# Performance work log

Hardware: AMD Instinct MI355X
Metric: run time of the kernel (lower is better)

Reference implementation:

```python
import jax, jax.numpy as jnp
import numpy as np
import math

B, S, D, N, H = 4, 2048, 1024, 512, 8
HD = D // H  # head_dim = 128
LN_EPS = 1e-5


def setup_inputs() -> dict:
    key = jax.random.key(0)
    ks = jax.random.split(key, 12)
    return {
        "query": jax.random.normal(ks[0], (B, S, D), jnp.float32),
        "memory_weights": jax.random.uniform(ks[1], (B, S, N), jnp.float32),
        "update_input": jax.random.normal(ks[2], (B, S, D), jnp.float32),
        "memory_keys": jax.random.normal(ks[3], (N, D), jnp.float32),
        "memory_values": jax.random.normal(ks[4], (N, D), jnp.float32),
        "memory_decay": jnp.float32(0.95),
        "gate_w": jax.random.normal(ks[5], (2 * D, D), jnp.float32) / math.sqrt(2 * D),
        "gate_b": jnp.zeros((D,), jnp.float32),
        "out_w": jax.random.normal(ks[6], (D, D), jnp.float32) / math.sqrt(D),
        "out_b": jnp.zeros((D,), jnp.float32),
        "ln_gamma": jnp.ones((D,), jnp.float32),
        "ln_beta": jnp.zeros((D,), jnp.float32),
    }


def reference(query, memory_weights, update_input, memory_keys, memory_values,
              memory_decay, gate_w, gate_b, out_w, out_b, ln_gamma, ln_beta):
    # Multi-head attention read: einsum 'bshd,nhd->bsn' sums over h and d,
    # so it equals a full [D]-dot product; only the scale uses head_dim.
    scores = jnp.einsum("bsd,nd->bsn", query, memory_keys) / math.sqrt(HD)
    scores = scores * memory_weights  # multiplicative mask before softmax
    probs = jax.nn.softmax(scores, axis=-1)
    memory_read = jnp.einsum("bsn,nd->bsd", probs, memory_values)
    memory_read = memory_read * memory_decay

    # Gated update path (update_input provided)
    gate_in = jnp.concatenate([memory_read, update_input], axis=-1)  # [B,S,2D]
    gate = jax.nn.sigmoid(gate_in @ gate_w + gate_b)  # [B,S,D]
    # NOTE: the no_grad EMA update of memory_values is a side effect that does
    # not influence this forward output; omitted from the pure reference.
    memory_read = memory_read * (1.0 + jnp.mean(gate, axis=-1, keepdims=True))

    out = memory_read @ out_w + out_b  # output projection (dropout = eval identity)
    mu = jnp.mean(out, axis=-1, keepdims=True)
    var = jnp.var(out, axis=-1, keepdims=True)
    out = (out - mu) * jax.lax.rsqrt(var + LN_EPS) * ln_gamma + ln_beta
    return out
```

## Files before the change

kernel.cpp:

```cpp
#include <hip/hip_runtime.h>
#include <hip/hip_bf16.h>

typedef __attribute__((ext_vector_type(8))) short bf16x8;
typedef __attribute__((ext_vector_type(4))) float f32x4;
typedef __attribute__((ext_vector_type(4))) int i32x4;
typedef __attribute__((ext_vector_type(2))) int i32x2;
typedef __attribute__((ext_vector_type(4))) unsigned short u16x4;

static __device__ __forceinline__ void gload_lds16(const void* g, void* l) {
  __builtin_amdgcn_global_load_lds((const __attribute__((address_space(1))) void*)g,
                                   (__attribute__((address_space(3))) void*)l,
                                   16, 0, 0);
}

static __device__ __forceinline__ unsigned short f2bf(float x) {
  unsigned int u = __float_as_uint(x);
  u += 0x7fffu + ((u >> 16) & 1u);
  return (unsigned short)(u >> 16);
}
static __device__ __forceinline__ float bf2f(unsigned short u) {
  return __uint_as_float((unsigned int)u << 16);
}

template <int BM, int BN, int NT>
static __device__ __forceinline__ void gemm_core(
    const unsigned short* __restrict__ A, int lda,
    const unsigned short* __restrict__ Bt, int ldb,
    int kbeg, int kend, int brow, int bcol,
    unsigned short* As, unsigned short* Bs,
    f32x4 (&acc)[BM / (8 * (NT / 64))][BN / 32])
{
  constexpr int NW = NT / 64;
  constexpr int MA = BM / (8 * NW), NB = BN / 32;
  constexpr int CA = 8 * BM / NT, CB = 8 * BN / NT;
  const int tid = threadIdx.x;
  const int wid = tid >> 6, lane = tid & 63;
  const int wr = wid >> 1, wc = wid & 1;
  const int l15 = lane & 15, l4 = lane >> 4;
  const int foff = tid * 8;

  for (int k0 = kbeg; k0 < kend; k0 += 64) {
#pragma unroll
    for (int c = 0; c < CA; ++c) {
      int f = c * (NT * 8) + foff;
      gload_lds16(A + (size_t)(brow + (f >> 6)) * lda + k0 + (f & 63), As + f);
    }
#pragma unroll
    for (int c = 0; c < CB; ++c) {
      int f = c * (NT * 8) + foff;
      gload_lds16(Bt + (size_t)(bcol + (f >> 6)) * ldb + k0 + (f & 63), Bs + f);
    }
    __syncthreads();
#pragma unroll
    for (int kk = 0; kk < 2; ++kk) {
      const int ko = kk * 32 + l4 * 8;
      bf16x8 af[MA], bfv[NB];
#pragma unroll
      for (int m = 0; m < MA; ++m)
        af[m] = *(const bf16x8*)(As + (wr * (16 * MA) + m * 16 + l15) * 64 + ko);
#pragma unroll
      for (int n = 0; n < NB; ++n)
        bfv[n] = *(const bf16x8*)(Bs + (wc * (BN / 2) + n * 16 + l15) * 64 + ko);
#pragma unroll
      for (int m = 0; m < MA; ++m)
#pragma unroll
        for (int n = 0; n < NB; ++n)
          acc[m][n] = __builtin_amdgcn_mfma_f32_16x16x32_bf16(af[m], bfv[n], acc[m][n], 0, 0, 0);
    }
    __syncthreads();
  }
}

__global__ __launch_bounds__(256)
void prep(const float* __restrict__ ob, int* __restrict__ flag,
          float* __restrict__ zeros,
          const float* __restrict__ mk, const float* __restrict__ mv,
          unsigned short* __restrict__ kb, unsigned short* __restrict__ mvb,
          const float* __restrict__ ow, unsigned short* __restrict__ owt,
          const float* __restrict__ q, unsigned short* __restrict__ qb,
          const float* __restrict__ upd, unsigned short* __restrict__ cat,
          const float* __restrict__ gw, unsigned short* __restrict__ gwt,
          unsigned short* __restrict__ vt)
{
  __shared__ float t[32][33];
  const int b = blockIdx.x;
  const int tid = threadIdx.x;
  if (b == 0) {
    f32x4 v = *(const f32x4*)(ob + tid * 4);
    float mx = fmaxf(fmaxf(fabsf(v[0]), fabsf(v[1])), fmaxf(fabsf(v[2]), fabsf(v[3])));
#pragma unroll
    for (int off = 32; off >= 1; off >>= 1) mx = fmaxf(mx, __shfl_xor(mx, off, 64));
    __shared__ float sm[4];
    const int wid = tid >> 6, lane = tid & 63;
    if (lane == 0) sm[wid] = mx;
    __syncthreads();
    if (tid == 0) {
      float m = fmaxf(fmaxf(sm[0], sm[1]), fmaxf(sm[2], sm[3]));
      *flag = (m != 0.0f) ? 1 : 0;
    }
  } else if (b < 17) {
    f32x4 z = {};
    *(f32x4*)(zeros + (b - 1) * 1024 + tid * 4) = z;
  } else if (b < 529) {
    int idx = (b - 17) * 256 + tid;
    const float* in; unsigned short* out; int rel;
    if (idx < 65536) { in = mk; out = kb;  rel = idx; }
    else             { in = mv; out = mvb; rel = idx - 65536; }
    size_t f = (size_t)rel * 8;
    f32x4 a = *(const f32x4*)(in + f);
    f32x4 c = *(const f32x4*)(in + f + 4);
    union { unsigned short u[8]; i32x4 vec; } pk;
#pragma unroll
    for (int i = 0; i < 4; ++i) { pk.u[i] = f2bf(a[i]); pk.u[4 + i] = f2bf(c[i]); }
    *(i32x4*)(out + f) = pk.vec;
  } else if (b < 1553) {
    int id = b - 529;
    const int bx = id & 31, by = id >> 5;
    const int tx = tid & 31, ty = tid >> 5;
    const int c0 = bx * 32, r0 = by * 32;
#pragma unroll
    for (int i = 0; i < 4; ++i)
      t[ty + i * 8][tx] = ow[(size_t)(r0 + ty + i * 8) * 1024 + c0 + tx];
    __syncthreads();
#pragma unroll
    for (int i = 0; i < 4; ++i)
      owt[(size_t)(c0 + ty + i * 8) * 1024 + r0 + tx] = f2bf(t[tx][ty + i * 8]);
  } else if (b < 5649) {
    int idx = (b - 1553) * 256 + tid;
    size_t f = (size_t)idx * 8;
    f32x4 a = *(const f32x4*)(q + f);
    f32x4 c = *(const f32x4*)(q + f + 4);
    union { unsigned short u[8]; i32x4 vec; } pk;
#pragma unroll
    for (int i = 0; i < 4; ++i) { pk.u[i] = f2bf(a[i]); pk.u[4 + i] = f2bf(c[i]); }
    *(i32x4*)(qb + f) = pk.vec;
  } else {
    f32x4 v = *(const f32x4*)(ob + tid * 4);
    float mx = fmaxf(fmaxf(fabsf(v[0]), fabsf(v[1])), fmaxf(fabsf(v[2]), fabsf(v[3])));
#pragma unroll
    for (int off = 32; off >= 1; off >>= 1) mx = fmaxf(mx, __shfl_xor(mx, off, 64));
    __shared__ float sm2[4];
    const int wid = tid >> 6, lane = tid & 63;
    if (lane == 0) sm2[wid] = mx;
    __syncthreads();
    float m = fmaxf(fmaxf(sm2[0], sm2[1]), fmaxf(sm2[2], sm2[3]));
    if (m == 0.0f) return;
    __syncthreads();
    int g = b - 5649;
    if (g < 4096) {
      int idx = g * 256 + tid;
      size_t f = (size_t)idx * 8;
      int row = (int)(f >> 10);
      int col = (int)(f & 1023);
      f32x4 a = *(const f32x4*)(upd + f);
      f32x4 c = *(const f32x4*)(upd + f + 4);
      union { unsigned short u[8]; i32x4 vec; } pk;
#pragma unroll
      for (int i = 0; i < 4; ++i) { pk.u[i] = f2bf(a[i]); pk.u[4 + i] = f2bf(c[i]); }
      *(i32x4*)(cat + (size_t)row * 2048 + 1024 + col) = pk.vec;
    } else {
      const float* in; unsigned short* out; int R, id;
      if (g < 6144) { in = gw; out = gwt; R = 2048; id = g - 4096; }
      else          { in = mv; out = vt;  R = 512;  id = g - 6144; }
      const int bx = id & 31, by = id >> 5;
      const int tx = tid & 31, ty = tid >> 5;
      const int c0 = bx * 32, r0 = by * 32;
#pragma unroll
      for (int i = 0; i < 4; ++i)
        t[ty + i * 8][tx] = in[(size_t)(r0 + ty + i * 8) * 1024 + c0 + tx];
      __syncthreads();
#pragma unroll
      for (int i = 0; i < 4; ++i)
        out[(size_t)(c0 + ty + i * 8) * R + r0 + tx] = f2bf(t[tx][ty + i * 8]);
    }
  }
}

__global__ __launch_bounds__(512, 8)
void k_scores_w2(const unsigned short* __restrict__ qb,
                 const unsigned short* __restrict__ kb,
                 const float* __restrict__ mw,
                 unsigned short* __restrict__ probs,
                 const unsigned short* __restrict__ owt,
                 const unsigned short* __restrict__ mvb,
                 float* __restrict__ w2p)
{
  __shared__ unsigned short As[128 * 64];
  __shared__ unsigned short Bs[64 * 64];
  const int b = blockIdx.x;
  const int tid = threadIdx.x;
  const int wid = tid >> 6, lane = tid & 63;
  const int wr = wid >> 1, wc = wid & 1;
  const int l15 = lane & 15, l4 = lane >> 4;

  if (b < 512) {
    const int swz = (b & 7) * 64 + (b >> 3);
    const int bx = swz & 7, by = swz >> 3;
    const int brow = by * 128, bcol = bx * 64;
    f32x4 acc[2][2] = {};
    gemm_core<128, 64, 512>(qb, 1024, kb, 1024, 0, 1024, brow, bcol, As, Bs, acc);

#pragma unroll
    for (int m = 0; m < 2; ++m) {
#pragma unroll
      for (int j = 0; j < 4; ++j) {
        int row = brow + wr * 32 + m * 16 + l4 * 4 + j;
        const float* mwrow = mw + (size_t)row * 512;
#pragma unroll
        for (int n = 0; n < 2; ++n) {
          int col = bcol + wc * 32 + n * 16 + l15;
          float p = __expf(acc[m][n][j] * 0.08838834764831845f * mwrow[col]);
          float o = __shfl_xor(p, 1);
          if (!(lane & 1)) {
            unsigned int pw = (unsigned int)f2bf(p) | ((unsigned int)f2bf(o) << 16);
            *(unsigned int*)(probs + (size_t)row * 512 + col) = pw;
          }
        }
      }
    }
  } else {
    const int g = b - 512;
    const int bx = g & 7;
    const int by = (g >> 3) & 7;
    const int bz = g >> 6;
    const int brow = by * 128, bcol = bx * 64;
    f32x4 acc[2][2] = {};
    gemm_core<128, 64, 512>(owt, 1024, mvb, 1024, bz * 512, bz * 512 + 512,
                            brow, bcol, As, Bs, acc);
    float* dst = w2p + (size_t)bz * 524288;
#pragma unroll
    for (int m = 0; m < 2; ++m) {
      int row0 = brow + wr * 32 + m * 16 + l4 * 4;
#pragma unroll
      for (int j = 0; j < 4; ++j) {
#pragma unroll
        for (int n = 0; n < 2; ++n)
          dst[(size_t)(row0 + j) * 512 + bcol + wc * 32 + n * 16 + l15] = acc[m][n][j];
      }
    }
  }
}

__global__ __launch_bounds__(256)
void k_w2red_rowsum(const float* __restrict__ w2p, unsigned short* __restrict__ w2t,
                    const float* __restrict__ dec,
                    const unsigned short* __restrict__ probs,
                    float* __restrict__ rowsum,
                    const int* __restrict__ flag)
{
  const int b = blockIdx.x;
  const int tid = threadIdx.x;
  if (b < 512) {
    const int i = (b * 256 + tid) * 4;
    const float d = *dec;
    f32x4 s0 = *(const f32x4*)(w2p + i);
    f32x4 s1 = *(const f32x4*)(w2p + 524288 + i);
    union { unsigned short u[4]; i32x2 v; } pk;
#pragma unroll
    for (int j = 0; j < 4; ++j) pk.u[j] = f2bf((s0[j] + s1[j]) * d);
    *(i32x2*)(w2t + i) = pk.v;
  } else {
    if (*flag == 0) return;
    const int wid = tid >> 6, lane = tid & 63;
    const int row = (b - 512) * 4 + wid;
    bf16x8 v = *(const bf16x8*)(probs + (size_t)row * 512 + lane * 8);
    float s = 0.0f;
#pragma unroll
    for (int i = 0; i < 8; ++i) s += bf2f((unsigned short)v[i]);
#pragma unroll
    for (int off = 32; off >= 1; off >>= 1) s += __shfl_xor(s, off, 64);
    if (lane == 0) rowsum[row] = s;
  }
}

__global__ __launch_bounds__(512)
void k_out_read(const unsigned short* __restrict__ probs,
                const unsigned short* __restrict__ w2t,
                const float* __restrict__ rowsum,
                unsigned short* __restrict__ outpre,
                const unsigned short* __restrict__ vt,
                unsigned short* __restrict__ cat,
                const float* __restrict__ dec,
                const int* __restrict__ flag)
{
  __shared__ unsigned short As[128 * 64];
  __shared__ unsigned short Bs[128 * 64];
  const int b = blockIdx.x;
  const int tid = threadIdx.x;
  const int wid = tid >> 6, lane = tid & 63;
  const int wr = wid >> 1, wc = wid & 1;
  const int l15 = lane & 15, l4 = lane >> 4;

  if (b < 512) {
    const int swz = (b & 7) * 64 + (b >> 3);
    const int bx = swz & 7, by = swz >> 3;
    const int brow = by * 128, bcol = bx * 128;
    f32x4 acc[2][4] = {};
    gemm_core<128, 128, 512>(probs, 512, w2t, 512, 0, 512, brow, bcol, As, Bs, acc);
    const bool nf = (*flag != 0);
#pragma unroll
    for (int m = 0; m < 2; ++m) {
      int row0 = brow + wr * 32 + m * 16 + l4 * 4;
#pragma unroll
      for (int j = 0; j < 4; ++j) {
        int row = row0 + j;
        const float rscl = nf ? (1.0f / rowsum[row]) : 1.0f;
#pragma unroll
        for (int n = 0; n < 4; ++n) {
          int col = bcol + wc * 64 + n * 16 + l15;
          float v = acc[m][n][j] * rscl;
          float o = __shfl_xor(v, 1);
          if (!(lane & 1)) {
            unsigned int pw = (unsigned int)f2bf(v) | ((unsigned int)f2bf(o) << 16);
            *(unsigned int*)(outpre + (size_t)row * 1024 + col) = pw;
          }
        }
      }
    }
  } else {
    if (*flag == 0) return;
    const int f = b - 512;
    const int swz = (f & 7) * 64 + (f >> 3);
    const int bx = swz & 7, by = swz >> 3;
    const int brow = by * 128, bcol = bx * 128;
    f32x4 acc[2][4] = {};
    gemm_core<128, 128, 512>(probs, 512, vt, 512, 0, 512, brow, bcol, As, Bs, acc);
    const float d = *dec;
#pragma unroll
    for (int m = 0; m < 2; ++m) {
      int row0 = brow + wr * 32 + m * 16 + l4 * 4;
#pragma unroll
      for (int j = 0; j < 4; ++j) {
        int row = row0 + j;
        const float rscl = d / rowsum[row];
#pragma unroll
        for (int n = 0; n < 4; ++n) {
          int col = bcol + wc * 64 + n * 16 + l15;
          cat[(size_t)row * 2048 + col] = f2bf(acc[m][n][j] * rscl);
        }
      }
    }
  }
}

__global__ __launch_bounds__(256)
void k_gate(const unsigned short* __restrict__ cat,
            const unsigned short* __restrict__ gwt,
            const float* __restrict__ gb,
            float* __restrict__ gsum,
            const int* __restrict__ flag)
{
  if (*flag == 0) return;
  __shared__ unsigned short As[128 * 64];
  __shared__ unsigned short Bs[128 * 64];
  const int b = blockIdx.x;
  const int tid = threadIdx.x;
  const int wid = tid >> 6, lane = tid & 63;
  const int wr = wid >> 1, wc = wid & 1;
  const int l15 = lane & 15, l4 = lane >> 4;
  const int swz = (b & 7) * 64 + (b >> 3);
  const int bx = swz & 7, by = swz >> 3;
  const int brow = by * 128, bcol = bx * 128;
  f32x4 acc[4][4] = {};
  gemm_core<128, 128, 256>(cat, 2048, gwt, 2048, 0, 2048, brow, bcol, As, Bs, acc);
#pragma unroll
  for (int m = 0; m < 4; ++m) {
#pragma unroll
    for (int j = 0; j < 4; ++j) {
      float part = 0.0f;
#pragma unroll
      for (int n = 0; n < 4; ++n) {
        int col = bcol + wc * 64 + n * 16 + l15;
        float x = acc[m][n][j] + gb[col];
        part += 1.0f / (1.0f + __expf(-x));
      }
#pragma unroll
      for (int off = 1; off < 16; off <<= 1)
        part += __shfl_xor(part, off, 64);
      if (l15 == 0) {
        int row = brow + wr * 64 + m * 16 + l4 * 4 + j;
        atomicAdd(&gsum[row], part);
      }
    }
  }
}

__global__ __launch_bounds__(256)
void ln_rows(const unsigned short* __restrict__ X, const float* __restrict__ gsum,
             const float* __restrict__ ob,
             const float* __restrict__ gamma, const float* __restrict__ beta,
             float* __restrict__ Y)
{
  const int row = blockIdx.x;
  const int tid = threadIdx.x;
  const size_t base = (size_t)row * 1024 + tid * 4;
  const float scl = 1.0f + gsum[row] * (1.0f / 1024.0f);
  u16x4 xr = *(const u16x4*)(X + base);
  f32x4 bo = *(const f32x4*)(ob + tid * 4);
  float x[4];
#pragma unroll
  for (int i = 0; i < 4; ++i) x[i] = bf2f(xr[i]) * scl + bo[i];
  float s = x[0] + x[1] + x[2] + x[3];
  float q = x[0] * x[0] + x[1] * x[1] + x[2] * x[2] + x[3] * x[3];
#pragma unroll
  for (int off = 32; off >= 1; off >>= 1) {
    s += __shfl_xor(s, off, 64);
    q += __shfl_xor(q, off, 64);
  }
  __shared__ float ss[4], qq[4];
  const int wid = tid >> 6, lane = tid & 63;
  if (lane == 0) { ss[wid] = s; qq[wid] = q; }
  __syncthreads();
  s = ss[0] + ss[1] + ss[2] + ss[3];
  q = qq[0] + qq[1] + qq[2] + qq[3];
  const float mu = s * (1.0f / 1024.0f);
  const float var = q * (1.0f / 1024.0f) - mu * mu;
  const float r = rsqrtf(var + 1e-5f);
  f32x4 g = *(const f32x4*)(gamma + tid * 4);
  f32x4 bt = *(const f32x4*)(beta + tid * 4);
  f32x4 y;
#pragma unroll
  for (int i = 0; i < 4; ++i) y[i] = (x[i] - mu) * r * g[i] + bt[i];
  *(f32x4*)(Y + base) = y;
}

extern "C" void kernel_launch(void* const* d_in, const int* in_sizes, int n_in,
                              void* d_out, int out_size, void* d_ws, size_t ws_size,
                              hipStream_t stream)
{
  (void)in_sizes; (void)n_in; (void)out_size; (void)ws_size;
  const float* q   = (const float*)d_in[0];
  const float* mw  = (const float*)d_in[1];
  const float* upd = (const float*)d_in[2];
  const float* mk  = (const float*)d_in[3];
  const float* mv  = (const float*)d_in[4];
  const float* dec = (const float*)d_in[5];
  const float* gw  = (const float*)d_in[6];
  const float* gb  = (const float*)d_in[7];
  const float* ow  = (const float*)d_in[8];
  const float* ob  = (const float*)d_in[9];
  const float* lg  = (const float*)d_in[10];
  const float* lb  = (const float*)d_in[11];
  float* outp = (float*)d_out;
  char* ws = (char*)d_ws;

  unsigned short* qb     = (unsigned short*)(ws + 0);
  unsigned short* probs  = (unsigned short*)(ws + 16777216);
  unsigned short* outpre = (unsigned short*)(ws + 25165824);
  unsigned short* kb     = (unsigned short*)(ws + 41943040);
  unsigned short* mvb    = (unsigned short*)(ws + 42991616);
  unsigned short* owt    = (unsigned short*)(ws + 44040192);
  unsigned short* w2t    = (unsigned short*)(ws + 46137344);
  float*          w2p    = (float*)(ws + 47185920);
  unsigned short* vt     = (unsigned short*)(ws + 51380224);
  unsigned short* gwt    = (unsigned short*)(ws + 52428800);
  unsigned short* cat    = (unsigned short*)(ws + 56623104);
  float*          gsum   = (float*)(ws + 90177536);
  float*          rowsum = (float*)(ws + 90210304);
  int*            flag   = (int*)(ws + 90243072);

  prep<<<12305, 256, 0, stream>>>(ob, flag, gsum, mk, mv, kb, mvb, ow, owt,
                                  q, qb, upd, cat, gw, gwt, vt);
  k_scores_w2<<<640, 512, 0, stream>>>(qb, kb, mw, probs, owt, mvb, w2p);
  k_w2red_rowsum<<<2560, 256, 0, stream>>>(w2p, w2t, dec, probs, rowsum, flag);
  k_out_read<<<1024, 512, 0, stream>>>(probs, w2t, rowsum, outpre, vt, cat, dec, flag);
  k_gate<<<512, 256, 0, stream>>>(cat, gwt, gb, gsum, flag);
  ln_rows<<<8192, 256, 0, stream>>>(outpre, gsum, ob, lg, lb, outp);
}
```

Before: 77.49 us.

## Drop split-K W2 reduction kernel, fuse rowsum into output GEMM, warp-per-row LayerNorm

The W2 = out_w^T·mem_values GEMM now runs over the full K range in 64 blocks instead of split-K into two fp32 partials. The decay-scaled bf16 result is written straight from the epilogue, which removes the separate reduction kernel and its launch. The probs row sums are recomputed inside each k_out_read block into shared memory rather than read from a global buffer. That adds redundant reads of probs (each row is summed by 8 column blocks). LayerNorm is restructured to one wavefront per row, removing the shared-memory reduction and block barrier.

```diff
diff --git a/kernel.cpp b/kernel.cpp
--- a/kernel.cpp
+++ b/kernel.cpp
@@ -5,7 +5,6 @@
 typedef __attribute__((ext_vector_type(4))) float f32x4;
 typedef __attribute__((ext_vector_type(4))) int i32x4;
 typedef __attribute__((ext_vector_type(2))) int i32x2;
-typedef __attribute__((ext_vector_type(4))) unsigned short u16x4;
 
 static __device__ __forceinline__ void gload_lds16(const void* g, void* l) {
   __builtin_amdgcn_global_load_lds((const __attribute__((address_space(1))) void*)g,
@@ -183,7 +182,8 @@
                  unsigned short* __restrict__ probs,
                  const unsigned short* __restrict__ owt,
                  const unsigned short* __restrict__ mvb,
-                 float* __restrict__ w2p)
+                 unsigned short* __restrict__ w2t,
+                 const float* __restrict__ dec)
 {
   __shared__ unsigned short As[128 * 64];
   __shared__ unsigned short Bs[64 * 64];
@@ -221,62 +221,34 @@
   } else {
     const int g = b - 512;
     const int bx = g & 7;
-    const int by = (g >> 3) & 7;
-    const int bz = g >> 6;
+    const int by = g >> 3;
     const int brow = by * 128, bcol = bx * 64;
     f32x4 acc[2][2] = {};
-    gemm_core<128, 64, 512>(owt, 1024, mvb, 1024, bz * 512, bz * 512 + 512,
-                            brow, bcol, As, Bs, acc);
-    float* dst = w2p + (size_t)bz * 524288;
+    gemm_core<128, 64, 512>(owt, 1024, mvb, 1024, 0, 1024, brow, bcol, As, Bs, acc);
+    const float d = *dec;
 #pragma unroll
     for (int m = 0; m < 2; ++m) {
-      int row0 = brow + wr * 32 + m * 16 + l4 * 4;
 #pragma unroll
       for (int j = 0; j < 4; ++j) {
-#pragma unroll
-        for (int n = 0; n < 2; ++n)
-          dst[(size_t)(row0 + j) * 512 + bcol + wc * 32 + n * 16 + l15] = acc[m][n][j];
-      }
-    }
-  }
-}
-
-__global__ __launch_bounds__(256)
-void k_w2red_rowsum(const float* __restrict__ w2p, unsigned short* __restrict__ w2t,
-                    const float* __restrict__ dec,
-                    const unsigned short* __restrict__ probs,
-                    float* __restrict__ rowsum,
-                    const int* __restrict__ flag)
-{
-  const int b = blockIdx.x;
-  const int tid = threadIdx.x;
-  if (b < 512) {
-    const int i = (b * 256 + tid) * 4;
-    const float d = *dec;
-    f32x4 s0 = *(const f32x4*)(w2p + i);
-    f32x4 s1 = *(const f32x4*)(w2p + 524288 + i);
-    union { unsigned short u[4]; i32x2 v; } pk;
-#pragma unroll
-    for (int j = 0; j < 4; ++j) pk.u[j] = f2bf((s0[j] + s1[j]) * d);
-    *(i32x2*)(w2t + i) = pk.v;
-  } else {
-    if (*flag == 0) return;
-    const int wid = tid >> 6, lane = tid & 63;
-    const int row = (b - 512) * 4 + wid;
-    bf16x8 v = *(const bf16x8*)(probs + (size_t)row * 512 + lane * 8);
-    float s = 0.0f;
-#pragma unroll
-    for (int i = 0; i < 8; ++i) s += bf2f((unsigned short)v[i]);
-#pragma unroll
-    for (int off = 32; off >= 1; off >>= 1) s += __shfl_xor(s, off, 64);
-    if (lane == 0) rowsum[row] = s;
+        int row = brow + wr * 32 + m * 16 + l4 * 4 + j;
+#pragma unroll
+        for (int n = 0; n < 2; ++n) {
+          int col = bcol + wc * 32 + n * 16 + l15;
+          float v = acc[m][n][j] * d;
+          float o = __shfl_xor(v, 1);
+          if (!(lane & 1)) {
+            unsigned int pw = (unsigned int)f2bf(v) | ((unsigned int)f2bf(o) << 16);
+            *(unsigned int*)(w2t + (size_t)row * 512 + col) = pw;
+          }
+        }
+      }
+    }
   }
 }
 
 __global__ __launch_bounds__(512)
 void k_out_read(const unsigned short* __restrict__ probs,
                 const unsigned short* __restrict__ w2t,
-                const float* __restrict__ rowsum,
                 unsigned short* __restrict__ outpre,
                 const unsigned short* __restrict__ vt,
                 unsigned short* __restrict__ cat,
@@ -285,11 +257,13 @@
 {
   __shared__ unsigned short As[128 * 64];
   __shared__ unsigned short Bs[128 * 64];
+  __shared__ float srow[128];
   const int b = blockIdx.x;
   const int tid = threadIdx.x;
   const int wid = tid >> 6, lane = tid & 63;
   const int wr = wid >> 1, wc = wid & 1;
   const int l15 = lane & 15, l4 = lane >> 4;
+  const bool nf = (*flag != 0);
 
   if (b < 512) {
     const int swz = (b & 7) * 64 + (b >> 3);
@@ -297,14 +271,26 @@
     const int brow = by * 128, bcol = bx * 128;
     f32x4 acc[2][4] = {};
     gemm_core<128, 128, 512>(probs, 512, w2t, 512, 0, 512, brow, bcol, As, Bs, acc);
-    const bool nf = (*flag != 0);
+    if (nf) {
+      for (int r = 0; r < 16; ++r) {
+        int row = brow + wid * 16 + r;
+        bf16x8 v = *(const bf16x8*)(probs + (size_t)row * 512 + lane * 8);
+        float s = 0.0f;
+#pragma unroll
+        for (int i = 0; i < 8; ++i) s += bf2f((unsigned short)v[i]);
+#pragma unroll
+        for (int off = 32; off >= 1; off >>= 1) s += __shfl_xor(s, off, 64);
+        if (lane == 0) srow[wid * 16 + r] = s;
+      }
+      __syncthreads();
+    }
 #pragma unroll
     for (int m = 0; m < 2; ++m) {
       int row0 = brow + wr * 32 + m * 16 + l4 * 4;
 #pragma unroll
       for (int j = 0; j < 4; ++j) {
         int row = row0 + j;
-        const float rscl = nf ? (1.0f / rowsum[row]) : 1.0f;
+        const float rscl = nf ? (1.0f / srow[row - brow]) : 1.0f;
 #pragma unroll
         for (int n = 0; n < 4; ++n) {
           int col = bcol + wc * 64 + n * 16 + l15;
@@ -318,13 +304,24 @@
       }
     }
   } else {
-    if (*flag == 0) return;
+    if (!nf) return;
     const int f = b - 512;
     const int swz = (f & 7) * 64 + (f >> 3);
     const int bx = swz & 7, by = swz >> 3;
     const int brow = by * 128, bcol = bx * 128;
     f32x4 acc[2][4] = {};
     gemm_core<128, 128, 512>(probs, 512, vt, 512, 0, 512, brow, bcol, As, Bs, acc);
+    for (int r = 0; r < 16; ++r) {
+      int row = brow + wid * 16 + r;
+      bf16x8 v = *(const bf16x8*)(probs + (size_t)row * 512 + lane * 8);
+      float s = 0.0f;
+#pragma unroll
+      for (int i = 0; i < 8; ++i) s += bf2f((unsigned short)v[i]);
+#pragma unroll
+      for (int off = 32; off >= 1; off >>= 1) s += __shfl_xor(s, off, 64);
+      if (lane == 0) srow[wid * 16 + r] = s;
+    }
+    __syncthreads();
     const float d = *dec;
 #pragma unroll
     for (int m = 0; m < 2; ++m) {
@@ -332,7 +329,7 @@
 #pragma unroll
       for (int j = 0; j < 4; ++j) {
         int row = row0 + j;
-        const float rscl = d / rowsum[row];
+        const float rscl = d / srow[row - brow];
 #pragma unroll
         for (int n = 0; n < 4; ++n) {
           int col = bcol + wc * 64 + n * 16 + l15;
@@ -391,37 +388,40 @@
              const float* __restrict__ gamma, const float* __restrict__ beta,
              float* __restrict__ Y)
 {
-  const int row = blockIdx.x;
-  const int tid = threadIdx.x;
-  const size_t base = (size_t)row * 1024 + tid * 4;
+  const int wid = threadIdx.x >> 6, lane = threadIdx.x & 63;
+  const int row = blockIdx.x * 4 + wid;
+  const size_t base = (size_t)row * 1024 + lane * 16;
+  const int cb = lane * 16;
   const float scl = 1.0f + gsum[row] * (1.0f / 1024.0f);
-  u16x4 xr = *(const u16x4*)(X + base);
-  f32x4 bo = *(const f32x4*)(ob + tid * 4);
-  float x[4];
-#pragma unroll
-  for (int i = 0; i < 4; ++i) x[i] = bf2f(xr[i]) * scl + bo[i];
-  float s = x[0] + x[1] + x[2] + x[3];
-  float q = x[0] * x[0] + x[1] * x[1] + x[2] * x[2] + x[3] * x[3];
+  bf16x8 x0 = *(const bf16x8*)(X + base);
+  bf16x8 x1 = *(const bf16x8*)(X + base + 8);
+  float x[16];
+#pragma unroll
+  for (int i = 0; i < 8; ++i) {
+    x[i]     = bf2f((unsigned short)x0[i]) * scl + ob[cb + i];
+    x[8 + i] = bf2f((unsigned short)x1[i]) * scl + ob[cb + 8 + i];
+  }
+  float s = 0.0f, qsum = 0.0f;
+#pragma unroll
+  for (int i = 0; i < 16; ++i) { s += x[i]; qsum += x[i] * x[i]; }
 #pragma unroll
   for (int off = 32; off >= 1; off >>= 1) {
     s += __shfl_xor(s, off, 64);
-    q += __shfl_xor(q, off, 64);
-  }
-  __shared__ float ss[4], qq[4];
-  const int wid = tid >> 6, lane = tid & 63;
-  if (lane == 0) { ss[wid] = s; qq[wid] = q; }
-  __syncthreads();
-  s = ss[0] + ss[1] + ss[2] + ss[3];
-  q = qq[0] + qq[1] + qq[2] + qq[3];
+    qsum += __shfl_xor(qsum, off, 64);
+  }
   const float mu = s * (1.0f / 1024.0f);
-  const float var = q * (1.0f / 1024.0f) - mu * mu;
+  const float var = qsum * (1.0f / 1024.0f) - mu * mu;
   const float r = rsqrtf(var + 1e-5f);
-  f32x4 g = *(const f32x4*)(gamma + tid * 4);
-  f32x4 bt = *(const f32x4*)(beta + tid * 4);
   f32x4 y;
 #pragma unroll
-  for (int i = 0; i < 4; ++i) y[i] = (x[i] - mu) * r * g[i] + bt[i];
-  *(f32x4*)(Y + base) = y;
+  for (int v4 = 0; v4 < 4; ++v4) {
+    f32x4 g = *(const f32x4*)(gamma + cb + v4 * 4);
+    f32x4 bt = *(const f32x4*)(beta + cb + v4 * 4);
+#pragma unroll
+    for (int i = 0; i < 4; ++i)
+      y[i] = (x[v4 * 4 + i] - mu) * r * g[i] + bt[i];
+    *(f32x4*)(Y + base + v4 * 4) = y;
+  }
 }
 
 extern "C" void kernel_launch(void* const* d_in, const int* in_sizes, int n_in,
@@ -451,19 +451,17 @@
   unsigned short* mvb    = (unsigned short*)(ws + 42991616);
   unsigned short* owt    = (unsigned short*)(ws + 44040192);
   unsigned short* w2t    = (unsigned short*)(ws + 46137344);
-  float*          w2p    = (float*)(ws + 47185920);
-  unsigned short* vt     = (unsigned short*)(ws + 51380224);
-  unsigned short* gwt    = (unsigned short*)(ws + 52428800);
-  unsigned short* cat    = (unsigned short*)(ws + 56623104);
-  float*          gsum   = (float*)(ws + 90177536);
-  float*          rowsum = (float*)(ws + 90210304);
-  int*            flag   = (int*)(ws + 90243072);
+  unsigned short* vt     = (unsigned short*)(ws + 47185920);
+  unsigned short* gwt    = (unsigned short*)(ws + 48234496);
+  unsigned short* cat    = (unsigned short*)(ws + 52428800);
+  float*          gsum   = (float*)(ws + 85983232);
+  float*          rowsum = (float*)(ws + 86016000);
+  int*            flag   = (int*)(ws + 86048768);
 
   prep<<<12305, 256, 0, stream>>>(ob, flag, gsum, mk, mv, kb, mvb, ow, owt,
                                   q, qb, upd, cat, gw, gwt, vt);
-  k_scores_w2<<<640, 512, 0, stream>>>(qb, kb, mw, probs, owt, mvb, w2p);
-  k_w2red_rowsum<<<2560, 256, 0, stream>>>(w2p, w2t, dec, probs, rowsum, flag);
-  k_out_read<<<1024, 512, 0, stream>>>(probs, w2t, rowsum, outpre, vt, cat, dec, flag);
+  k_scores_w2<<<576, 512, 0, stream>>>(qb, kb, mw, probs, owt, mvb, w2t, dec);
+  k_out_read<<<1024, 512, 0, stream>>>(probs, w2t, outpre, vt, cat, dec, flag);
   k_gate<<<512, 256, 0, stream>>>(cat, gwt, gb, gsum, flag);
-  ln_rows<<<8192, 256, 0, stream>>>(outpre, gsum, ob, lg, lb, outp);
-}
+  ln_rows<<<2048, 256, 0, stream>>>(outpre, gsum, ob, lg, lb, outp);
+}
```

Result: slower. 85.55 us, median of 2 (+10.4%).

## Rebalance kernel stages: move memory-read GEMM earlier and fuse gate GEMM with output

Applied to the files above, without the earlier changes.

The probs×V memory-read GEMM moves into the earlier w2 reduction/rowsum kernel. It computes its own per-tile row sums in shared memory instead of waiting for the global rowsum. The gate GEMM is then co-scheduled with the output GEMM in one launch, which drops a kernel launch and the serialization between the read and gate stages. The trade-offs are that the moved GEMM now runs in 256-thread blocks with 128x128 tiles and more accumulators per thread, and that each block recomputes row sums redundantly.

```diff
diff --git a/kernel.cpp b/kernel.cpp
--- a/kernel.cpp
+++ b/kernel.cpp
@@ -242,12 +242,18 @@
 }
 
 __global__ __launch_bounds__(256)
-void k_w2red_rowsum(const float* __restrict__ w2p, unsigned short* __restrict__ w2t,
-                    const float* __restrict__ dec,
-                    const unsigned short* __restrict__ probs,
-                    float* __restrict__ rowsum,
-                    const int* __restrict__ flag)
-{
+void k_w2red_rows_read(const float* __restrict__ w2p,
+                       unsigned short* __restrict__ w2t,
+                       const float* __restrict__ dec,
+                       const unsigned short* __restrict__ probs,
+                       float* __restrict__ rowsum,
+                       const unsigned short* __restrict__ vt,
+                       unsigned short* __restrict__ cat,
+                       const int* __restrict__ flag)
+{
+  __shared__ unsigned short As[128 * 64];
+  __shared__ unsigned short Bs[128 * 64];
+  __shared__ float srow[128];
   const int b = blockIdx.x;
   const int tid = threadIdx.x;
   if (b < 512) {
@@ -259,7 +265,7 @@
 #pragma unroll
     for (int j = 0; j < 4; ++j) pk.u[j] = f2bf((s0[j] + s1[j]) * d);
     *(i32x2*)(w2t + i) = pk.v;
-  } else {
+  } else if (b < 2560) {
     if (*flag == 0) return;
     const int wid = tid >> 6, lane = tid & 63;
     const int row = (b - 512) * 4 + wid;
@@ -270,17 +276,55 @@
 #pragma unroll
     for (int off = 32; off >= 1; off >>= 1) s += __shfl_xor(s, off, 64);
     if (lane == 0) rowsum[row] = s;
+  } else {
+    if (*flag == 0) return;
+    const int f = b - 2560;
+    const int swz = (f & 7) * 64 + (f >> 3);
+    const int bx = swz & 7, by = swz >> 3;
+    const int brow = by * 128, bcol = bx * 128;
+    const int wid = tid >> 6, lane = tid & 63;
+    const int wr = wid >> 1, wc = wid & 1;
+    const int l15 = lane & 15, l4 = lane >> 4;
+    f32x4 acc[4][4] = {};
+    gemm_core<128, 128, 256>(probs, 512, vt, 512, 0, 512, brow, bcol, As, Bs, acc);
+    for (int r = 0; r < 32; ++r) {
+      int lrow = wid * 32 + r;
+      bf16x8 v = *(const bf16x8*)(probs + (size_t)(brow + lrow) * 512 + lane * 8);
+      float s = 0.0f;
+#pragma unroll
+      for (int i = 0; i < 8; ++i) s += bf2f((unsigned short)v[i]);
+#pragma unroll
+      for (int off = 32; off >= 1; off >>= 1) s += __shfl_xor(s, off, 64);
+      if (lane == 0) srow[lrow] = s;
+    }
+    __syncthreads();
+    const float d = *dec;
+#pragma unroll
+    for (int m = 0; m < 4; ++m) {
+      int row0 = brow + wr * 64 + m * 16 + l4 * 4;
+#pragma unroll
+      for (int j = 0; j < 4; ++j) {
+        int row = row0 + j;
+        const float rscl = d / srow[row - brow];
+#pragma unroll
+        for (int n = 0; n < 4; ++n) {
+          int col = bcol + wc * 64 + n * 16 + l15;
+          cat[(size_t)row * 2048 + col] = f2bf(acc[m][n][j] * rscl);
+        }
+      }
+    }
   }
 }
 
 __global__ __launch_bounds__(512)
-void k_out_read(const unsigned short* __restrict__ probs,
+void k_out_gate(const unsigned short* __restrict__ probs,
                 const unsigned short* __restrict__ w2t,
                 const float* __restrict__ rowsum,
                 unsigned short* __restrict__ outpre,
-                const unsigned short* __restrict__ vt,
-                unsigned short* __restrict__ cat,
-                const float* __restrict__ dec,
+                const unsigned short* __restrict__ cat,
+                const unsigned short* __restrict__ gwt,
+                const float* __restrict__ gb,
+                float* __restrict__ gsum,
                 const int* __restrict__ flag)
 {
   __shared__ unsigned short As[128 * 64];
@@ -324,62 +368,25 @@
     const int bx = swz & 7, by = swz >> 3;
     const int brow = by * 128, bcol = bx * 128;
     f32x4 acc[2][4] = {};
-    gemm_core<128, 128, 512>(probs, 512, vt, 512, 0, 512, brow, bcol, As, Bs, acc);
-    const float d = *dec;
+    gemm_core<128, 128, 512>(cat, 2048, gwt, 2048, 0, 2048, brow, bcol, As, Bs, acc);
 #pragma unroll
     for (int m = 0; m < 2; ++m) {
-      int row0 = brow + wr * 32 + m * 16 + l4 * 4;
 #pragma unroll
       for (int j = 0; j < 4; ++j) {
-        int row = row0 + j;
-        const float rscl = d / rowsum[row];
+        float part = 0.0f;
 #pragma unroll
         for (int n = 0; n < 4; ++n) {
           int col = bcol + wc * 64 + n * 16 + l15;
-          cat[(size_t)row * 2048 + col] = f2bf(acc[m][n][j] * rscl);
+          float x = acc[m][n][j] + gb[col];
+          part += 1.0f / (1.0f + __expf(-x));
         }
-      }
-    }
-  }
-}
-
-__global__ __launch_bounds__(256)
-void k_gate(const unsigned short* __restrict__ cat,
-            const unsigned short* __restrict__ gwt,
-            const float* __restrict__ gb,
-            float* __restrict__ gsum,
-            const int* __restrict__ flag)
-{
-  if (*flag == 0) return;
-  __shared__ unsigned short As[128 * 64];
-  __shared__ unsigned short Bs[128 * 64];
-  const int b = blockIdx.x;
-  const int tid = threadIdx.x;
-  const int wid = tid >> 6, lane = tid & 63;
-  const int wr = wid >> 1, wc = wid & 1;
-  const int l15 = lane & 15, l4 = lane >> 4;
-  const int swz = (b & 7) * 64 + (b >> 3);
-  const int bx = swz & 7, by = swz >> 3;
-  const int brow = by * 128, bcol = bx * 128;
-  f32x4 acc[4][4] = {};
-  gemm_core<128, 128, 256>(cat, 2048, gwt, 2048, 0, 2048, brow, bcol, As, Bs, acc);
-#pragma unroll
-  for (int m = 0; m < 4; ++m) {
-#pragma unroll
-    for (int j = 0; j < 4; ++j) {
-      float part = 0.0f;
-#pragma unroll
-      for (int n = 0; n < 4; ++n) {
-        int col = bcol + wc * 64 + n * 16 + l15;
-        float x = acc[m][n][j] + gb[col];
-        part += 1.0f / (1.0f + __expf(-x));
-      }
-#pragma unroll
-      for (int off = 1; off < 16; off <<= 1)
-        part += __shfl_xor(part, off, 64);
-      if (l15 == 0) {
-        int row = brow + wr * 64 + m * 16 + l4 * 4 + j;
-        atomicAdd(&gsum[row], part);
+#pragma unroll
+        for (int off = 1; off < 16; off <<= 1)
+          part += __shfl_xor(part, off, 64);
+        if (l15 == 0) {
+          int row = brow + wr * 32 + m * 16 + l4 * 4 + j;
+          atomicAdd(&gsum[row], part);
+        }
       }
     }
   }
@@ -462,8 +469,9 @@
   prep<<<12305, 256, 0, stream>>>(ob, flag, gsum, mk, mv, kb, mvb, ow, owt,
                                   q, qb, upd, cat, gw, gwt, vt);
   k_scores_w2<<<640, 512, 0, stream>>>(qb, kb, mw, probs, owt, mvb, w2p);
-  k_w2red_rowsum<<<2560, 256, 0, stream>>>(w2p, w2t, dec, probs, rowsum, flag);
-  k_out_read<<<1024, 512, 0, stream>>>(probs, w2t, rowsum, outpre, vt, cat, dec, flag);
-  k_gate<<<512, 256, 0, stream>>>(cat, gwt, gb, gsum, flag);
+  k_w2red_rows_read<<<3072, 256, 0, stream>>>(w2p, w2t, dec, probs, rowsum,
+                                              vt, cat, flag);
+  k_out_gate<<<1024, 512, 0, stream>>>(probs, w2t, rowsum, outpre, cat, gwt,
+                                       gb, gsum, flag);
   ln_rows<<<8192, 256, 0, stream>>>(outpre, gsum, ob, lg, lb, outp);
 }
```

New measurement: 76.97 us (median of 2 runs). About the same (-0.7%).
